# Kernel optimization log

Measured on AMD Instinct MI355X. Metric: run time of the kernel, lower is better.

## Reference

```python
import jax, jax.numpy as jnp
import numpy as np

N, D, E, H, K = 8192, 1024, 8, 256, 2


def setup_inputs() -> dict:
    key = jax.random.key(0)
    ks = jax.random.split(key, 9)
    s = 0.02
    return {
        "x": jax.random.normal(ks[0], (N, D), dtype=jnp.float32),
        "Wg": jax.random.normal(ks[1], (D, E), dtype=jnp.float32) * s,
        "bg": jnp.zeros((E,), dtype=jnp.float32),
        "W1": jax.random.normal(ks[2], (E, D, H), dtype=jnp.float32) * s,
        "b1": jnp.zeros((E, H), dtype=jnp.float32),
        "W2": jax.random.normal(ks[3], (E, H, H), dtype=jnp.float32) * s,
        "b2": jnp.zeros((E, H), dtype=jnp.float32),
        "W3": jax.random.normal(ks[4], (E, H, D), dtype=jnp.float32) * s,
        "b3": jnp.zeros((E, D), dtype=jnp.float32),
    }


def reference(x, Wg, bg, W1, b1, W2, b2, W3, b3):
    # Gating: softmax over experts, then keep only top-k gate values per token.
    gates = jax.nn.softmax(x @ Wg + bg, axis=-1)              # [N, E]
    top_v, top_i = jax.lax.top_k(gates, K)                    # [N, K]
    rows = jnp.arange(gates.shape[0])[:, None]                # [N, 1]
    top_k_gates = jnp.zeros_like(gates).at[rows, top_i].set(top_v)  # [N, E]

    # Dense all-expert MLP (matches original: every expert runs on every token).
    h = jax.nn.relu(jnp.einsum('nd,edh->neh', x, W1) + b1)    # [N, E, H]
    h = jax.nn.relu(jnp.einsum('neh,ehg->neg', h, W2) + b2)   # [N, E, H]  (dropout is eval no-op)
    eo = jax.nn.relu(jnp.einsum('neh,ehd->ned', h, W3) + b3)  # [N, E, D]

    # Combine with masked gates: einsum('...nde,...ne->...nd') with eo in 'ned' layout.
    output = jnp.einsum('ned,ne->nd', eo, top_k_gates)        # [N, D]
    return output
```

## Files before the change

kernel.cpp:

```cpp
#include <hip/hip_runtime.h>
#include <math.h>

#define NTOK 8192
#define DDIM 1024
#define NEXP 8
#define HDIM 256
#define TOPK 2
#define PADM 128
#define CAPS (NTOK * TOPK + NEXP * PADM)
#define NT128 (CAPS / 128)

typedef __attribute__((ext_vector_type(8))) __bf16 bf16x8;
typedef __attribute__((ext_vector_type(4))) float f32x4;

#define GLDS16(g, s)                                                      \
    __builtin_amdgcn_global_load_lds(                                     \
        (const __attribute__((address_space(1))) void*)(g),               \
        (__attribute__((address_space(3))) void*)(s), 16, 0, 0)

static constexpr size_t OFF_TOFF = 128;
static constexpr size_t OFF_ZBUF = 4096;
static constexpr size_t OFF_T2E  = 8192;
static constexpr size_t OFF_T2G  = OFF_T2E + (size_t)NTOK * TOPK * 4;
static constexpr size_t OFF_SLOT = OFF_T2G + (size_t)NTOK * TOPK * 4;
static constexpr size_t OFF_TOK  = OFF_SLOT + (size_t)NTOK * TOPK * 4;
static constexpr size_t OFF_GAT  = OFF_TOK + (size_t)CAPS * 4;
static constexpr size_t OFF_XB   = (OFF_GAT + (size_t)CAPS * 4 + 255) & ~(size_t)255;
static constexpr size_t OFF_W1T  = OFF_XB  + (size_t)NTOK * DDIM * 2;
static constexpr size_t OFF_W2T  = OFF_W1T + (size_t)NEXP * DDIM * HDIM * 2;
static constexpr size_t OFF_W3T  = OFF_W2T + (size_t)NEXP * HDIM * HDIM * 2;
static constexpr size_t OFF_H1   = OFF_W3T + (size_t)NEXP * HDIM * DDIM * 2;
static constexpr size_t OFF_H2   = OFF_H1  + (size_t)CAPS * HDIM * 2;
static constexpr size_t OFF_H3   = OFF_H2  + (size_t)CAPS * HDIM * 2;

static __device__ __forceinline__ unsigned short f2b(float f) {
    __bf16 h = (__bf16)f;
    return __builtin_bit_cast(unsigned short, h);
}
static __device__ __forceinline__ float b2f(unsigned short u) {
    return __builtin_bit_cast(float, ((unsigned)u) << 16);
}

__global__ __launch_bounds__(256) void gate_trans(
    const float* __restrict__ x, const float* __restrict__ Wg,
    const float* __restrict__ bg, unsigned short* __restrict__ xb,
    int* __restrict__ top2e, float* __restrict__ top2g,
    const float* __restrict__ W1, const float* __restrict__ W2,
    const float* __restrict__ W3, __bf16* __restrict__ w1t,
    __bf16* __restrict__ w2t, __bf16* __restrict__ w3t)
{
    __shared__ __align__(16) float sh[NEXP * DDIM];
    const int tid = threadIdx.x;

    if (blockIdx.x < 256) {
        for (int d = tid; d < DDIM; d += 256) {
            const float4 w0 = *(const float4*)(Wg + (size_t)d * NEXP);
            const float4 w1 = *(const float4*)(Wg + (size_t)d * NEXP + 4);
            sh[0 * DDIM + d] = w0.x; sh[1 * DDIM + d] = w0.y;
            sh[2 * DDIM + d] = w0.z; sh[3 * DDIM + d] = w0.w;
            sh[4 * DDIM + d] = w1.x; sh[5 * DDIM + d] = w1.y;
            sh[6 * DDIM + d] = w1.z; sh[7 * DDIM + d] = w1.w;
        }
        __syncthreads();

        const int n = (blockIdx.y * 256 + blockIdx.x) * 4 + (tid >> 6);
        const int lane = tid & 63;
        const float* xr = x + (size_t)n * DDIM;
        unsigned short* xbr = xb + (size_t)n * DDIM;

        float acc[NEXP];
#pragma unroll
        for (int e = 0; e < NEXP; ++e) acc[e] = 0.f;

#pragma unroll
        for (int it = 0; it < 4; ++it) {
            const int d = it * 256 + lane * 4;
            const float4 xv = *(const float4*)(xr + d);
            ushort4 u;
            u.x = f2b(xv.x); u.y = f2b(xv.y); u.z = f2b(xv.z); u.w = f2b(xv.w);
            *(ushort4*)(xbr + d) = u;
#pragma unroll
            for (int e = 0; e < NEXP; ++e) {
                const float4 wt = *(const float4*)(sh + e * DDIM + d);
                acc[e] = fmaf(xv.x, wt.x, acc[e]);
                acc[e] = fmaf(xv.y, wt.y, acc[e]);
                acc[e] = fmaf(xv.z, wt.z, acc[e]);
                acc[e] = fmaf(xv.w, wt.w, acc[e]);
            }
        }
#pragma unroll
        for (int off = 32; off > 0; off >>= 1)
#pragma unroll
            for (int e = 0; e < NEXP; ++e) acc[e] += __shfl_down(acc[e], off, 64);

        if (lane == 0) {
            float v[NEXP], mx = -1e30f;
#pragma unroll
            for (int e = 0; e < NEXP; ++e) { v[e] = acc[e] + bg[e]; mx = fmaxf(mx, v[e]); }
            float p[NEXP], s = 0.f;
#pragma unroll
            for (int e = 0; e < NEXP; ++e) { p[e] = expf(v[e] - mx); s += p[e]; }
            const float inv = 1.f / s;
#pragma unroll
            for (int e = 0; e < NEXP; ++e) p[e] *= inv;
            int i0 = 0;
#pragma unroll
            for (int e = 1; e < NEXP; ++e) if (p[e] > p[i0]) i0 = e;
            int i1 = (i0 == 0) ? 1 : 0;
#pragma unroll
            for (int e = 0; e < NEXP; ++e) if (e != i0 && p[e] > p[i1]) i1 = e;
            top2e[n * 2 + 0] = i0;  top2e[n * 2 + 1] = i1;
            top2g[n * 2 + 0] = p[i0]; top2g[n * 2 + 1] = p[i1];
        }
    } else {
        const int e = blockIdx.y;
        int bt = blockIdx.x - 256;
        const float* Wi; __bf16* Wo; int R, C, xt, yt;
        if (bt < 256)      { Wi = W1; Wo = w1t; R = DDIM; C = HDIM; xt = bt & 7;  yt = bt >> 3; }
        else if (bt < 320) { bt -= 256; Wi = W2; Wo = w2t; R = HDIM; C = HDIM; xt = bt & 7;  yt = bt >> 3; }
        else               { bt -= 320; Wi = W3; Wo = w3t; R = HDIM; C = DDIM; xt = bt & 31; yt = bt >> 5; }
        const int r0 = yt * 32, c0 = xt * 32;
        const int tx = tid & 31, ty = tid >> 5;
        const float* Wie = Wi + (size_t)e * R * C;
        __bf16* Woe = Wo + (size_t)e * C * R;
#pragma unroll
        for (int j = 0; j < 4; ++j)
            sh[(ty + j * 8) * 33 + tx] = Wie[(size_t)(r0 + ty + j * 8) * C + c0 + tx];
        __syncthreads();
#pragma unroll
        for (int j = 0; j < 4; ++j)
            Woe[(size_t)(c0 + ty + j * 8) * R + r0 + tx] = (__bf16)sh[tx * 33 + ty + j * 8];
    }
}

__global__ __launch_bounds__(1024) void route(
    const int* __restrict__ top2e, const float* __restrict__ top2g,
    int* __restrict__ toff, int* __restrict__ tok, float* __restrict__ gat,
    int* __restrict__ slotof, float* __restrict__ zbuf)
{
    const int tid = threadIdx.x;
    const int wv = tid >> 6, ln = tid & 63;
    __shared__ int   waveTot[16][NEXP];
    __shared__ int   waveBase[16][NEXP];
    __shared__ int   totS[NEXP];
    __shared__ int   toffS[NEXP + 1];
    __shared__ short excS[1024][NEXP];

    zbuf[tid] = 0.f;

    int myE[16]; float myG[16];
    const int4*   pe = (const int4*)(top2e + tid * 16);
    const float4* pg = (const float4*)(top2g + tid * 16);
#pragma unroll
    for (int q = 0; q < 4; ++q) {
        const int4 v = pe[q];
        myE[q * 4 + 0] = v.x; myE[q * 4 + 1] = v.y;
        myE[q * 4 + 2] = v.z; myE[q * 4 + 3] = v.w;
        const float4 g = pg[q];
        myG[q * 4 + 0] = g.x; myG[q * 4 + 1] = g.y;
        myG[q * 4 + 2] = g.z; myG[q * 4 + 3] = g.w;
    }

#pragma unroll
    for (int e = 0; e < NEXP; ++e) {
        int c = 0;
#pragma unroll
        for (int j = 0; j < 16; ++j) c += (myE[j] == e);
        int inc = c;
#pragma unroll
        for (int off = 1; off < 64; off <<= 1) {
            const int t = __shfl_up(inc, off, 64);
            if (ln >= off) inc += t;
        }
        excS[tid][e] = (short)(inc - c);
        if (ln == 63) waveTot[wv][e] = inc;
    }
    __syncthreads();

    if (tid < NEXP) {
        int b = 0;
#pragma unroll
        for (int w = 0; w < 16; ++w) {
            const int t = waveTot[w][tid];
            waveBase[w][tid] = b;
            b += t;
        }
        totS[tid] = b;
    }
    __syncthreads();

    if (tid == 0) {
        int acc = 0;
#pragma unroll
        for (int e = 0; e < NEXP; ++e) {
            toffS[e] = acc;
            acc += (totS[e] + PADM - 1) & ~(PADM - 1);
        }
        toffS[NEXP] = acc;
#pragma unroll
        for (int e = 0; e <= NEXP; ++e) toff[e] = toffS[e];
    }
    __syncthreads();

#pragma unroll
    for (int j = 0; j < 16; ++j) {
        int pre = 0;
#pragma unroll
        for (int j2 = 0; j2 < j; ++j2) pre += (myE[j2] == myE[j]);
        const int e = myE[j];
        const int slot = toffS[e] + waveBase[wv][e] + (int)excS[tid][e] + pre;
        const int i = tid * 16 + j;
        tok[slot] = i >> 1;
        gat[slot] = myG[j];
        slotof[i] = slot;
    }

#pragma unroll
    for (int e = 0; e < NEXP; ++e) {
        const int begin = toffS[e] + totS[e];
        const int end   = toffS[e + 1];
        for (int i = begin + tid; i < end; i += 1024) {
            tok[i] = -1;
            gat[i] = 0.f;
        }
    }
}

template<int KDIM, int NCOL, bool GATHER, bool FINAL>
__global__ __launch_bounds__(256) void egemm(
    const __bf16* __restrict__ Ain, const __bf16* __restrict__ Wt,
    const float* __restrict__ ball, const int* __restrict__ toff,
    const int* __restrict__ tok, const float* __restrict__ gat,
    const char* __restrict__ zbuf, __bf16* __restrict__ Out)
{
    const int total = toff[NEXP];
    const int slot0 = blockIdx.x * 128;
    if (slot0 >= total) return;
    int e = 0;
    while (toff[e + 1] <= slot0) ++e;
    const int col0 = blockIdx.y * 128;

    __shared__ __align__(16) char smem[32768];
    char* AsB = smem;
    char* BsB = smem + 16384;

    const int tid  = threadIdx.x;
    const int lane = tid & 63;
    const int wid  = tid >> 6;
    const int wr = wid >> 1, wc = wid & 1;

    const int srow  = tid >> 3;
    const int sslot = tid & 7;
    const __bf16* We = Wt + (size_t)e * NCOL * KDIM;
    const char* ap[4];
    const char* bp[4];
#pragma unroll
    for (int i = 0; i < 4; ++i) {
        const int row = i * 32 + srow;
        const int ks  = sslot ^ (row & 7);
        if (GATHER) {
            const int t = tok[slot0 + row];
            ap[i] = (t >= 0) ? (const char*)(Ain + (size_t)t * KDIM + ks * 8) : zbuf;
        } else {
            ap[i] = (const char*)(Ain + (size_t)(slot0 + row) * KDIM + ks * 8);
        }
        bp[i] = (const char*)(We + (size_t)(col0 + row) * KDIM + ks * 8);
    }

    const int llo = lane & 15, lhi = lane >> 4;
    int abyte[4], am7[4], bbyte[4], bm7[4];
#pragma unroll
    for (int m = 0; m < 4; ++m) {
        const int r = wr * 64 + m * 16 + llo;
        abyte[m] = r * 128; am7[m] = r & 7;
        const int c = wc * 64 + m * 16 + llo;
        bbyte[m] = c * 128; bm7[m] = c & 7;
    }

    f32x4 acc[4][4];
#pragma unroll
    for (int m = 0; m < 4; ++m)
#pragma unroll
        for (int n = 0; n < 4; ++n) acc[m][n] = (f32x4){0.f, 0.f, 0.f, 0.f};

    for (int k0 = 0; k0 < KDIM; k0 += 64) {
        const size_t kb = (size_t)k0 * 2;
#pragma unroll
        for (int i = 0; i < 4; ++i)
            GLDS16(ap[i] + kb, AsB + i * 4096 + wid * 1024);
#pragma unroll
        for (int i = 0; i < 4; ++i)
            GLDS16(bp[i] + kb, BsB + i * 4096 + wid * 1024);
        __syncthreads();
#pragma unroll
        for (int kk = 0; kk < 2; ++kk) {
            bf16x8 af[4], bfr[4];
#pragma unroll
            for (int m = 0; m < 4; ++m)
                af[m] = *(const bf16x8*)(AsB + abyte[m] + ((((kk << 2) + lhi) ^ am7[m]) << 4));
#pragma unroll
            for (int n = 0; n < 4; ++n)
                bfr[n] = *(const bf16x8*)(BsB + bbyte[n] + ((((kk << 2) + lhi) ^ bm7[n]) << 4));
#pragma unroll
            for (int m = 0; m < 4; ++m)
#pragma unroll
                for (int n = 0; n < 4; ++n)
                    acc[m][n] = __builtin_amdgcn_mfma_f32_16x16x32_bf16(
                        af[m], bfr[n], acc[m][n], 0, 0, 0);
        }
        __syncthreads();
    }

    const float* be = ball + (size_t)e * NCOL;
#pragma unroll
    for (int m = 0; m < 4; ++m) {
        const int rbase = slot0 + wr * 64 + m * 16 + lhi * 4;
        float g[4];
        if (FINAL) {
#pragma unroll
            for (int j = 0; j < 4; ++j) g[j] = gat[rbase + j];
        }
#pragma unroll
        for (int n = 0; n < 4; ++n) {
            const int col = col0 + wc * 64 + n * 16 + llo;
            const float bb = be[col];
#pragma unroll
            for (int j = 0; j < 4; ++j) {
                float v = fmaxf(acc[m][n][j] + bb, 0.f);
                if (FINAL) v *= g[j];
                Out[(size_t)(rbase + j) * NCOL + col] = (__bf16)v;
            }
        }
    }
}

__global__ __launch_bounds__(256) void combine(
    const unsigned short* __restrict__ h3, const int* __restrict__ slotof,
    float* __restrict__ out)
{
    const int n = blockIdx.x;
    const int c = threadIdx.x * 4;
    const int s0 = slotof[n * 2], s1 = slotof[n * 2 + 1];
    const ushort4 a = *(const ushort4*)(h3 + (size_t)s0 * DDIM + c);
    const ushort4 b = *(const ushort4*)(h3 + (size_t)s1 * DDIM + c);
    float4 o;
    o.x = b2f(a.x) + b2f(b.x);
    o.y = b2f(a.y) + b2f(b.y);
    o.z = b2f(a.z) + b2f(b.z);
    o.w = b2f(a.w) + b2f(b.w);
    *(float4*)(out + (size_t)n * DDIM + c) = o;
}

extern "C" void kernel_launch(void* const* d_in, const int* in_sizes, int n_in,
                              void* d_out, int out_size, void* d_ws, size_t ws_size,
                              hipStream_t stream)
{
    const float* x  = (const float*)d_in[0];
    const float* Wg = (const float*)d_in[1];
    const float* bg = (const float*)d_in[2];
    const float* W1 = (const float*)d_in[3];
    const float* b1 = (const float*)d_in[4];
    const float* W2 = (const float*)d_in[5];
    const float* b2 = (const float*)d_in[6];
    const float* W3 = (const float*)d_in[7];
    const float* b3 = (const float*)d_in[8];
    float* out = (float*)d_out;

    char* ws = (char*)d_ws;
    int*   toff   = (int*)(ws + OFF_TOFF);
    char*  zbuf   = ws + OFF_ZBUF;
    int*   top2e  = (int*)(ws + OFF_T2E);
    float* top2g  = (float*)(ws + OFF_T2G);
    int*   slotof = (int*)(ws + OFF_SLOT);
    int*   tok    = (int*)(ws + OFF_TOK);
    float* gat    = (float*)(ws + OFF_GAT);
    unsigned short* xbu = (unsigned short*)(ws + OFF_XB);
    __bf16* xb  = (__bf16*)(ws + OFF_XB);
    __bf16* w1t = (__bf16*)(ws + OFF_W1T);
    __bf16* w2t = (__bf16*)(ws + OFF_W2T);
    __bf16* w3t = (__bf16*)(ws + OFF_W3T);
    __bf16* h1  = (__bf16*)(ws + OFF_H1);
    __bf16* h2  = (__bf16*)(ws + OFF_H2);
    __bf16* h3  = (__bf16*)(ws + OFF_H3);

    gate_trans<<<dim3(832, NEXP), 256, 0, stream>>>(
        x, Wg, bg, xbu, top2e, top2g, W1, W2, W3, w1t, w2t, w3t);
    route<<<1, 1024, 0, stream>>>(top2e, top2g, toff, tok, gat, slotof, (float*)zbuf);

    egemm<DDIM, HDIM, true,  false><<<dim3(NT128, HDIM / 128), 256, 0, stream>>>(
        xb, w1t, b1, toff, tok, gat, zbuf, h1);
    egemm<HDIM, HDIM, false, false><<<dim3(NT128, HDIM / 128), 256, 0, stream>>>(
        h1, w2t, b2, toff, tok, gat, zbuf, h2);
    egemm<HDIM, DDIM, false, true ><<<dim3(NT128, DDIM / 128), 256, 0, stream>>>(
        h2, w3t, b3, toff, tok, gat, zbuf, h3);

    combine<<<NTOK, 256, 0, stream>>>((const unsigned short*)h3, slotof, out);
}
```

Measured before the change: 108.1 us.

## Fuse first two expert GEMMs keeping h1 in shared memory

Merges the first and second expert MLP layers into one kernel. Each block computes a 64-row by 256-column h1 tile, stores it swizzled in LDS, then multiplies it by W2 directly, so h1 is never written to or read back from global memory. The third GEMM's grid is reordered so that column tiles vary fastest, which is meant to improve reuse of A rows in cache. The fused kernel uses 72KB of LDS and a smaller M tile, which lowers occupancy and gives less reuse of the W1 loads.

```diff
diff --git a/kernel.cpp b/kernel.cpp
--- a/kernel.cpp
+++ b/kernel.cpp
@@ -8,6 +8,7 @@
 #define TOPK 2
 #define PADM 128
 #define CAPS (NTOK * TOPK + NEXP * PADM)
+#define NT64  (CAPS / 64)
 #define NT128 (CAPS / 128)
 
 typedef __attribute__((ext_vector_type(8))) __bf16 bf16x8;
@@ -29,8 +30,7 @@
 static constexpr size_t OFF_W1T  = OFF_XB  + (size_t)NTOK * DDIM * 2;
 static constexpr size_t OFF_W2T  = OFF_W1T + (size_t)NEXP * DDIM * HDIM * 2;
 static constexpr size_t OFF_W3T  = OFF_W2T + (size_t)NEXP * HDIM * HDIM * 2;
-static constexpr size_t OFF_H1   = OFF_W3T + (size_t)NEXP * HDIM * DDIM * 2;
-static constexpr size_t OFF_H2   = OFF_H1  + (size_t)CAPS * HDIM * 2;
+static constexpr size_t OFF_H2   = OFF_W3T + (size_t)NEXP * HDIM * DDIM * 2;
 static constexpr size_t OFF_H3   = OFF_H2  + (size_t)CAPS * HDIM * 2;
 
 static __device__ __forceinline__ unsigned short f2b(float f) {
@@ -226,19 +226,171 @@
     }
 }
 
-template<int KDIM, int NCOL, bool GATHER, bool FINAL>
-__global__ __launch_bounds__(256) void egemm(
-    const __bf16* __restrict__ Ain, const __bf16* __restrict__ Wt,
-    const float* __restrict__ ball, const int* __restrict__ toff,
-    const int* __restrict__ tok, const float* __restrict__ gat,
-    const char* __restrict__ zbuf, __bf16* __restrict__ Out)
+__global__ __launch_bounds__(256) void egemm12(
+    const __bf16* __restrict__ xb, const __bf16* __restrict__ w1t,
+    const __bf16* __restrict__ w2t, const float* __restrict__ b1,
+    const float* __restrict__ b2, const int* __restrict__ toff,
+    const int* __restrict__ tok, const char* __restrict__ zbuf,
+    __bf16* __restrict__ h2)
 {
     const int total = toff[NEXP];
-    const int slot0 = blockIdx.x * 128;
+    const int slot0 = blockIdx.x * 64;
     if (slot0 >= total) return;
     int e = 0;
     while (toff[e + 1] <= slot0) ++e;
-    const int col0 = blockIdx.y * 128;
+
+    __shared__ __align__(16) char smem[73728];
+    char* AsB = smem;
+    char* BsB = smem + 8192;
+    char* H1s = smem + 40960;
+
+    const int tid  = threadIdx.x;
+    const int lane = tid & 63;
+    const int wid  = tid >> 6;
+
+    const int srow  = tid >> 3;
+    const int sslot = tid & 7;
+    const int ks    = sslot ^ (srow & 7);
+
+    const __bf16* We1 = w1t + (size_t)e * HDIM * DDIM;
+    const char* ap[2];
+#pragma unroll
+    for (int i = 0; i < 2; ++i) {
+        const int t = tok[slot0 + i * 32 + srow];
+        ap[i] = (t >= 0) ? (const char*)(xb + (size_t)t * DDIM + ks * 8) : zbuf;
+    }
+    const char* bp1[8];
+#pragma unroll
+    for (int i = 0; i < 8; ++i)
+        bp1[i] = (const char*)(We1 + (size_t)(i * 32 + srow) * DDIM + ks * 8);
+
+    const int llo = lane & 15, lhi = lane >> 4;
+    const int m7 = llo & 7;
+    int abyte[4], bbyte[4];
+#pragma unroll
+    for (int m = 0; m < 4; ++m) {
+        abyte[m] = (m * 16 + llo) * 128;
+        bbyte[m] = (wid * 64 + m * 16 + llo) * 128;
+    }
+
+    f32x4 acc[4][4];
+#pragma unroll
+    for (int m = 0; m < 4; ++m)
+#pragma unroll
+        for (int n = 0; n < 4; ++n) acc[m][n] = (f32x4){0.f, 0.f, 0.f, 0.f};
+
+    for (int k0 = 0; k0 < DDIM; k0 += 64) {
+        const size_t kb = (size_t)k0 * 2;
+        GLDS16(ap[0] + kb, AsB + tid * 16);
+        GLDS16(ap[1] + kb, AsB + 4096 + tid * 16);
+#pragma unroll
+        for (int i = 0; i < 8; ++i)
+            GLDS16(bp1[i] + kb, BsB + i * 4096 + tid * 16);
+        __syncthreads();
+#pragma unroll
+        for (int kk = 0; kk < 2; ++kk) {
+            const int sl = ((kk << 2) + lhi) ^ m7;
+            bf16x8 af[4], bfr[4];
+#pragma unroll
+            for (int m = 0; m < 4; ++m) af[m]  = *(const bf16x8*)(AsB + abyte[m] + (sl << 4));
+#pragma unroll
+            for (int n = 0; n < 4; ++n) bfr[n] = *(const bf16x8*)(BsB + bbyte[n] + (sl << 4));
+#pragma unroll
+            for (int m = 0; m < 4; ++m)
+#pragma unroll
+                for (int n = 0; n < 4; ++n)
+                    acc[m][n] = __builtin_amdgcn_mfma_f32_16x16x32_bf16(
+                        af[m], bfr[n], acc[m][n], 0, 0, 0);
+        }
+        __syncthreads();
+    }
+
+    {
+        const float* be1 = b1 + (size_t)e * HDIM;
+#pragma unroll
+        for (int n = 0; n < 4; ++n) {
+            const int col = wid * 64 + n * 16 + llo;
+            const float bb = be1[col];
+            const int colbyte = (col & 7) * 2;
+            const int slice = col >> 3;
+#pragma unroll
+            for (int m = 0; m < 4; ++m) {
+#pragma unroll
+                for (int j = 0; j < 4; ++j) {
+                    const int r = m * 16 + lhi * 4 + j;
+                    const float v = fmaxf(acc[m][n][j] + bb, 0.f);
+                    *(__bf16*)(H1s + r * 512 + ((slice ^ (r & 7)) << 4) + colbyte) = (__bf16)v;
+                }
+                acc[m][n] = (f32x4){0.f, 0.f, 0.f, 0.f};
+            }
+        }
+    }
+    __syncthreads();
+
+    const __bf16* We2 = w2t + (size_t)e * HDIM * HDIM;
+    const char* bp2[8];
+#pragma unroll
+    for (int i = 0; i < 8; ++i)
+        bp2[i] = (const char*)(We2 + (size_t)(i * 32 + srow) * HDIM + ks * 8);
+
+    for (int k2 = 0; k2 < 4; ++k2) {
+        const size_t kb = (size_t)k2 * 128;
+#pragma unroll
+        for (int i = 0; i < 8; ++i)
+            GLDS16(bp2[i] + kb, BsB + i * 4096 + tid * 16);
+        __syncthreads();
+#pragma unroll
+        for (int kk = 0; kk < 2; ++kk) {
+            const int slB = ((kk << 2) + lhi) ^ m7;
+            const int sA  = k2 * 8 + (kk << 2) + lhi;
+            const int slA = sA ^ m7;
+            bf16x8 af[4], bfr[4];
+#pragma unroll
+            for (int m = 0; m < 4; ++m)
+                af[m] = *(const bf16x8*)(H1s + (m * 16 + llo) * 512 + (slA << 4));
+#pragma unroll
+            for (int n = 0; n < 4; ++n)
+                bfr[n] = *(const bf16x8*)(BsB + bbyte[n] + (slB << 4));
+#pragma unroll
+            for (int m = 0; m < 4; ++m)
+#pragma unroll
+                for (int n = 0; n < 4; ++n)
+                    acc[m][n] = __builtin_amdgcn_mfma_f32_16x16x32_bf16(
+                        af[m], bfr[n], acc[m][n], 0, 0, 0);
+        }
+        __syncthreads();
+    }
+
+    {
+        const float* be2 = b2 + (size_t)e * HDIM;
+#pragma unroll
+        for (int n = 0; n < 4; ++n) {
+            const int col = wid * 64 + n * 16 + llo;
+            const float bb = be2[col];
+#pragma unroll
+            for (int m = 0; m < 4; ++m) {
+#pragma unroll
+                for (int j = 0; j < 4; ++j) {
+                    const int r = slot0 + m * 16 + lhi * 4 + j;
+                    h2[(size_t)r * HDIM + col] = (__bf16)fmaxf(acc[m][n][j] + bb, 0.f);
+                }
+            }
+        }
+    }
+}
+
+template<int KDIM, int NCOL>
+__global__ __launch_bounds__(256) void egemm3(
+    const __bf16* __restrict__ Ain, const __bf16* __restrict__ Wt,
+    const float* __restrict__ ball, const int* __restrict__ toff,
+    const float* __restrict__ gat, __bf16* __restrict__ Out)
+{
+    const int total = toff[NEXP];
+    const int slot0 = blockIdx.y * 128;
+    if (slot0 >= total) return;
+    int e = 0;
+    while (toff[e + 1] <= slot0) ++e;
+    const int col0 = blockIdx.x * 128;
 
     __shared__ __align__(16) char smem[32768];
     char* AsB = smem;
@@ -251,30 +403,24 @@
 
     const int srow  = tid >> 3;
     const int sslot = tid & 7;
+    const int ks    = sslot ^ (srow & 7);
     const __bf16* We = Wt + (size_t)e * NCOL * KDIM;
     const char* ap[4];
     const char* bp[4];
 #pragma unroll
     for (int i = 0; i < 4; ++i) {
         const int row = i * 32 + srow;
-        const int ks  = sslot ^ (row & 7);
-        if (GATHER) {
-            const int t = tok[slot0 + row];
-            ap[i] = (t >= 0) ? (const char*)(Ain + (size_t)t * KDIM + ks * 8) : zbuf;
-        } else {
-            ap[i] = (const char*)(Ain + (size_t)(slot0 + row) * KDIM + ks * 8);
-        }
+        ap[i] = (const char*)(Ain + (size_t)(slot0 + row) * KDIM + ks * 8);
         bp[i] = (const char*)(We + (size_t)(col0 + row) * KDIM + ks * 8);
     }
 
     const int llo = lane & 15, lhi = lane >> 4;
-    int abyte[4], am7[4], bbyte[4], bm7[4];
+    const int m7 = llo & 7;
+    int abyte[4], bbyte[4];
 #pragma unroll
     for (int m = 0; m < 4; ++m) {
-        const int r = wr * 64 + m * 16 + llo;
-        abyte[m] = r * 128; am7[m] = r & 7;
-        const int c = wc * 64 + m * 16 + llo;
-        bbyte[m] = c * 128; bm7[m] = c & 7;
+        abyte[m] = (wr * 64 + m * 16 + llo) * 128;
+        bbyte[m] = (wc * 64 + m * 16 + llo) * 128;
     }
 
     f32x4 acc[4][4];
@@ -294,13 +440,12 @@
         __syncthreads();
 #pragma unroll
         for (int kk = 0; kk < 2; ++kk) {
+            const int sl = ((kk << 2) + lhi) ^ m7;
             bf16x8 af[4], bfr[4];
 #pragma unroll
-            for (int m = 0; m < 4; ++m)
-                af[m] = *(const bf16x8*)(AsB + abyte[m] + ((((kk << 2) + lhi) ^ am7[m]) << 4));
-#pragma unroll
-            for (int n = 0; n < 4; ++n)
-                bfr[n] = *(const bf16x8*)(BsB + bbyte[n] + ((((kk << 2) + lhi) ^ bm7[n]) << 4));
+            for (int m = 0; m < 4; ++m) af[m]  = *(const bf16x8*)(AsB + abyte[m] + (sl << 4));
+#pragma unroll
+            for (int n = 0; n < 4; ++n) bfr[n] = *(const bf16x8*)(BsB + bbyte[n] + (sl << 4));
 #pragma unroll
             for (int m = 0; m < 4; ++m)
 #pragma unroll
@@ -316,18 +461,15 @@
     for (int m = 0; m < 4; ++m) {
         const int rbase = slot0 + wr * 64 + m * 16 + lhi * 4;
         float g[4];
-        if (FINAL) {
-#pragma unroll
-            for (int j = 0; j < 4; ++j) g[j] = gat[rbase + j];
-        }
+#pragma unroll
+        for (int j = 0; j < 4; ++j) g[j] = gat[rbase + j];
 #pragma unroll
         for (int n = 0; n < 4; ++n) {
             const int col = col0 + wc * 64 + n * 16 + llo;
             const float bb = be[col];
 #pragma unroll
             for (int j = 0; j < 4; ++j) {
-                float v = fmaxf(acc[m][n][j] + bb, 0.f);
-                if (FINAL) v *= g[j];
+                const float v = fmaxf(acc[m][n][j] + bb, 0.f) * g[j];
                 Out[(size_t)(rbase + j) * NCOL + col] = (__bf16)v;
             }
         }
@@ -379,7 +521,6 @@
     __bf16* w1t = (__bf16*)(ws + OFF_W1T);
     __bf16* w2t = (__bf16*)(ws + OFF_W2T);
     __bf16* w3t = (__bf16*)(ws + OFF_W3T);
-    __bf16* h1  = (__bf16*)(ws + OFF_H1);
     __bf16* h2  = (__bf16*)(ws + OFF_H2);
     __bf16* h3  = (__bf16*)(ws + OFF_H3);
 
@@ -387,12 +528,9 @@
         x, Wg, bg, xbu, top2e, top2g, W1, W2, W3, w1t, w2t, w3t);
     route<<<1, 1024, 0, stream>>>(top2e, top2g, toff, tok, gat, slotof, (float*)zbuf);
 
-    egemm<DDIM, HDIM, true,  false><<<dim3(NT128, HDIM / 128), 256, 0, stream>>>(
-        xb, w1t, b1, toff, tok, gat, zbuf, h1);
-    egemm<HDIM, HDIM, false, false><<<dim3(NT128, HDIM / 128), 256, 0, stream>>>(
-        h1, w2t, b2, toff, tok, gat, zbuf, h2);
-    egemm<HDIM, DDIM, false, true ><<<dim3(NT128, DDIM / 128), 256, 0, stream>>>(
-        h2, w3t, b3, toff, tok, gat, zbuf, h3);
+    egemm12<<<NT64, 256, 0, stream>>>(xb, w1t, w2t, b1, b2, toff, tok, zbuf, h2);
+    egemm3<HDIM, DDIM><<<dim3(DDIM / 128, NT128), 256, 0, stream>>>(
+        h2, w3t, b3, toff, gat, h3);
 
     combine<<<NTOK, 256, 0, stream>>>((const unsigned short*)h3, slotof, out);
 }
```

Result: no change. 106.8 us (-1.2%).
